# Kernel optimization log

Measured on AMD Instinct MI355X. Metric: run time of the kernel, lower is better.

## Reference

```python
import jax, jax.numpy as jnp
import numpy as np

S = 2   # upsample scale
K = 5   # reassembly kernel k_up


def setup_inputs() -> dict:
    key = jax.random.key(0)
    ks = jax.random.split(key, 7)
    B, C, H, W = 4, 128, 64, 64
    C_MID = 64
    return {
        "x": jax.random.normal(ks[0], (B, C, H, W), dtype=jnp.float32),
        "w1": jax.random.normal(ks[1], (C_MID, C), dtype=jnp.float32) * 0.05,
        "w2": jax.random.normal(ks[2], (S * S * K * K, C_MID, 3, 3), dtype=jnp.float32) * 0.05,
        "bn_gamma": jax.random.uniform(ks[3], (C_MID,), dtype=jnp.float32, minval=0.5, maxval=1.5),
        "bn_beta": jax.random.normal(ks[4], (C_MID,), dtype=jnp.float32) * 0.1,
        "bn_mean": jax.random.normal(ks[5], (C_MID,), dtype=jnp.float32) * 0.1,
        "bn_var": jax.random.uniform(ks[6], (C_MID,), dtype=jnp.float32, minval=0.5, maxval=1.5),
    }


def reference(x, w1, w2, bn_gamma, bn_beta, bn_mean, bn_var):
    B, C, H, W = x.shape
    s, k = S, K
    eps = 1e-5
    # --- content encoder: 1x1 conv -> BN (inference form) -> ReLU -> 3x3 conv ---
    h = jnp.einsum('bchw,oc->bohw', x, w1)  # (B, c_mid, H, W)
    inv = bn_gamma / jnp.sqrt(bn_var + eps)
    h = h * inv[None, :, None, None] + (bn_beta - bn_mean * inv)[None, :, None, None]
    h = jax.nn.relu(h)
    ker = jax.lax.conv_general_dilated(
        h, w2, window_strides=(1, 1), padding=((1, 1), (1, 1)),
        dimension_numbers=('NCHW', 'OIHW', 'NCHW'))  # (B, s*s*k*k, H, W)
    # softmax over the k*k reassembly window
    ker = jax.nn.softmax(ker.reshape(B, s * s, k * k, H, W), axis=2)
    # --- unfold k x k neighborhoods of x (row-major window order, as F.unfold) ---
    p = k // 2
    xp = jnp.pad(x, ((0, 0), (0, 0), (p, p), (p, p)))
    patches = jnp.stack(
        [xp[:, :, i:i + H, j:j + W] for i in range(k) for j in range(k)],
        axis=2)  # (B, C, k*k, H, W)
    # weighted reassembly: sum over the k*k window per (sub-pixel, channel)
    out = jnp.einsum('bckhw,bskhw->bcshw', patches, ker)  # (B, C, s*s, H, W)
    # pixel shuffle: (B, C, s, s, H, W) -> (B, C, H*s, W*s)
    out = out.reshape(B, C, s, s, H, W).transpose(0, 1, 4, 2, 5, 3)
    return out.reshape(B, C, H * s, W * s)
```

## Files before the change

kernel.cpp:

```cpp
#include <hip/hip_runtime.h>
#include <hip/hip_bf16.h>

#define HW 4096

typedef __attribute__((ext_vector_type(8))) short  short8;
typedef __attribute__((ext_vector_type(4))) float  floatx4;

#define OFF_W2B 0ul
#define OFF_W1B 129024ul
#define OFF_BN  145408ul
#define OFF_XG  145920ul

__device__ __forceinline__ float bfbits(unsigned u) {
    union { unsigned u; float f; } t; t.u = u; return t.f;
}

__global__ __launch_bounds__(256) void prep_kernel(const float* __restrict__ x,
                                                   const float* __restrict__ w1,
                                                   const float* __restrict__ w2,
                                                   const float* __restrict__ gamma,
                                                   const float* __restrict__ beta,
                                                   const float* __restrict__ mean,
                                                   const float* __restrict__ var,
                                                   char* __restrict__ ws) {
    int tid = blockIdx.x * 256 + threadIdx.x;
    if (tid < 262144) {
        int pix = tid & 4095;
        int cq  = (tid >> 12) & 15;
        int b   = tid >> 16;
        const float* xp = x + ((size_t)(b * 128 + cq * 8)) * HW + pix;
        union { short8 s; __hip_bfloat16 h[8]; } u;
        #pragma unroll
        for (int cc = 0; cc < 8; ++cc) u.h[cc] = __float2bfloat16(xp[(size_t)cc * HW]);
        *(short8*)((__hip_bfloat16*)(ws + OFF_XG) + (size_t)tid * 8) = u.s;
        return;
    }
    int t2 = tid - 262144;
    if (t2 < 64512) {
        int n = t2 / 576;
        int k = t2 - n * 576;
        int t = k >> 6, c = k & 63;
        float v = (n < 100) ? w2[(n * 64 + c) * 9 + t] : 0.f;
        ((__hip_bfloat16*)(ws + OFF_W2B))[t2] = __float2bfloat16(v);
    } else if (t2 < 64512 + 8192) {
        int i = t2 - 64512;
        ((__hip_bfloat16*)(ws + OFF_W1B))[i] = __float2bfloat16(w1[i]);
    } else if (t2 < 64512 + 8192 + 64) {
        int o = t2 - 64512 - 8192;
        float inv = gamma[o] * rsqrtf(var[o] + 1e-5f);
        ((float2*)(ws + OFF_BN))[o] = make_float2(inv, beta[o] - mean[o] * inv);
    }
}

__global__ __launch_bounds__(512, 4) void fused_carafe(const char* __restrict__ ws,
                                                       float* __restrict__ out) {
    __shared__ __align__(16) __hip_bfloat16 xs[1536 * 8];
    __shared__ __align__(16) __hip_bfloat16 hs[60 * 72];
    __shared__ __align__(16) float lg[32 * 114];
    __shared__ __align__(16) float ks[100 * 33];

    int b    = blockIdx.x >> 7;
    int tile = blockIdx.x & 127;
    int ty0 = (tile >> 3) * 4;
    int tx0 = (tile & 7) * 8;
    int tid = threadIdx.x;
    int lane = tid & 63, wave = tid >> 6;
    int q = lane >> 4, m = lane & 15;

    int bnt = wave & 3;
    int bo  = bnt * 16 + m;
    const __hip_bfloat16* w1b = (const __hip_bfloat16*)(ws + OFF_W1B);
    short8 bw[4];
    #pragma unroll
    for (int s = 0; s < 4; ++s)
        bw[s] = *(const short8*)(w1b + bo * 128 + s * 32 + q * 8);
    float2 bnia = ((const float2*)(ws + OFF_BN))[bo];

    const __hip_bfloat16* xg = (const __hip_bfloat16*)(ws + OFF_XG) + (size_t)b * 16 * 4096 * 8;
    #pragma unroll
    for (int it = 0; it < 3; ++it) {
        int idx = tid + it * 512;
        int cq = idx / 96, p = idx - cq * 96;
        int hy = p / 12, hx = p - hy * 12;
        int gy = ty0 + hy - 2, gx = tx0 + hx - 2;
        short8 v;
        #pragma unroll
        for (int j = 0; j < 8; ++j) v[j] = 0;
        if ((unsigned)gy < 64u && (unsigned)gx < 64u)
            v = *(const short8*)(xg + ((size_t)cq * 4096 + gy * 64 + gx) * 8);
        *(short8*)(&xs[idx * 8]) = v;
    }
    __syncthreads();

    #pragma unroll
    for (int mi = 0; mi < 2; ++mi) {
        int mt = (wave >> 2) * 2 + mi;
        int hp = mt * 16 + m;
        int hy1 = hp / 10, hx1 = hp - hy1 * 10;
        int xrow = (hy1 + 1) * 12 + (hx1 + 1);
        floatx4 acc;
        #pragma unroll
        for (int r = 0; r < 4; ++r) acc[r] = 0.f;
        #pragma unroll
        for (int s = 0; s < 4; ++s) {
            short8 a = *(const short8*)(&xs[((s * 4 + q) * 96 + xrow) * 8]);
            acc = __builtin_amdgcn_mfma_f32_16x16x32_bf16(a, bw[s], acc, 0, 0, 0);
        }
        #pragma unroll
        for (int r = 0; r < 4; ++r) {
            int prow = mt * 16 + q * 4 + r;
            if (prow < 60) {
                int phy = prow / 10, phx = prow - phy * 10;
                int gy = ty0 + phy - 1, gx = tx0 + phx - 1;
                bool in = ((unsigned)gy < 64u) && ((unsigned)gx < 64u);
                float v = in ? fmaxf(fmaf(acc[r], bnia.x, bnia.y), 0.f) : 0.f;
                hs[prow * 72 + bo] = __float2bfloat16(v);
            }
        }
    }
    __syncthreads();

    for (int task = wave; task < 14; task += 8) {
        int mt = task & 1, nt = task >> 1;
        int pixidx = mt * 16 + m;
        int py = pixidx >> 3, px = pixidx & 7;
        const __hip_bfloat16* w2b = (const __hip_bfloat16*)(ws + OFF_W2B);
        const __hip_bfloat16* bp  = w2b + (size_t)(nt * 16 + m) * 576 + q * 8;

        floatx4 acc;
        #pragma unroll
        for (int r = 0; r < 4; ++r) acc[r] = 0.f;

        short8 bcur = *(const short8*)bp;
        for (int s = 0; s < 18; ++s) {
            int t = s >> 1, c0 = (s & 1) * 32;
            int ti = t / 3, tj = t - ti * 3;
            short8 a = *(const short8*)(&hs[((py + ti) * 10 + px + tj) * 72 + c0 + q * 8]);
            short8 bn2 = bcur;
            if (s < 17) bn2 = *(const short8*)(bp + (s + 1) * 32);
            acc = __builtin_amdgcn_mfma_f32_16x16x32_bf16(a, bcur, acc, 0, 0, 0);
            bcur = bn2;
        }
        #pragma unroll
        for (int r = 0; r < 4; ++r)
            lg[(mt * 16 + q * 4 + r) * 114 + nt * 16 + m] = acc[r];
    }
    __syncthreads();

    if (tid < 128) {
        int pix = tid & 31, g = tid >> 5;
        float v[25];
        #pragma unroll
        for (int wi = 0; wi < 25; ++wi) v[wi] = lg[pix * 114 + g * 25 + wi];
        float mx = v[0];
        #pragma unroll
        for (int wi = 1; wi < 25; ++wi) mx = fmaxf(mx, v[wi]);
        float ssum = 0.f;
        #pragma unroll
        for (int wi = 0; wi < 25; ++wi) { v[wi] = __expf(v[wi] - mx); ssum += v[wi]; }
        float rs = 1.f / ssum;
        #pragma unroll
        for (int t25 = 0; t25 < 25; ++t25)
            ks[(t25 * 4 + g) * 33 + pix] = v[t25] * rs;
    }
    __syncthreads();

    {
        int pix   = lane & 31;
        int chunk = lane >> 5;
        int py = pix >> 3, px = pix & 7;
        int Y = ty0 + py, X = tx0 + px;

        for (int co = wave; co < 16; co += 8) {
            float acc[16];
            #pragma unroll
            for (int i = 0; i < 16; ++i) acc[i] = 0.f;

            const __hip_bfloat16* xsb = xs + (size_t)co * 96 * 8;
            #pragma unroll 5
            for (int t = 0; t < 25; ++t) {
                int ti = t / 5, tj = t - ti * 5;
                int xrow = (py + ti) * 12 + (px + tj);
                union { short8 s; unsigned u[4]; } xv;
                xv.s = *(const short8*)(xsb + xrow * 8);
                float k0 = ks[(t * 4 + chunk * 2 + 0) * 33 + pix];
                float k1 = ks[(t * 4 + chunk * 2 + 1) * 33 + pix];
                #pragma unroll
                for (int j = 0; j < 4; ++j) {
                    float xa  = bfbits(xv.u[j] << 16);
                    float xb2 = bfbits(xv.u[j] & 0xFFFF0000u);
                    acc[(j * 2 + 0) * 2 + 0] = fmaf(xa,  k0, acc[(j * 2 + 0) * 2 + 0]);
                    acc[(j * 2 + 0) * 2 + 1] = fmaf(xa,  k1, acc[(j * 2 + 0) * 2 + 1]);
                    acc[(j * 2 + 1) * 2 + 0] = fmaf(xb2, k0, acc[(j * 2 + 1) * 2 + 0]);
                    acc[(j * 2 + 1) * 2 + 1] = fmaf(xb2, k1, acc[(j * 2 + 1) * 2 + 1]);
                }
            }

            #pragma unroll
            for (int i = 0; i < 8; ++i) {
                size_t o0 = (((size_t)b * 128 + co * 8 + i) * 128 + 2 * Y + chunk) * 128 + 2 * X;
                *(float2*)(out + o0) = make_float2(acc[i * 2 + 0], acc[i * 2 + 1]);
            }
        }
    }
}

extern "C" void kernel_launch(void* const* d_in, const int* in_sizes, int n_in,
                              void* d_out, int out_size, void* d_ws, size_t ws_size,
                              hipStream_t stream) {
    const float* x     = (const float*)d_in[0];
    const float* w1    = (const float*)d_in[1];
    const float* w2    = (const float*)d_in[2];
    const float* gamma = (const float*)d_in[3];
    const float* beta  = (const float*)d_in[4];
    const float* mean  = (const float*)d_in[5];
    const float* var   = (const float*)d_in[6];
    float* out = (float*)d_out;
    char*  ws  = (char*)d_ws;

    prep_kernel<<<1309, 256, 0, stream>>>(x, w1, w2, gamma, beta, mean, var, ws);
    fused_carafe<<<512, 512, 0, stream>>>(ws, out);
}
```

Baseline: 102.2 us.

## Shrink output tile to 4x4, alias shared buffers, double blocks per CU

Changes the spatial tile from 4x8 to 4x4 pixels and launches 1024 blocks instead of 512. Shared memory is packed into one aliased buffer (hs and ks overlap) so occupancy can rise to 8 blocks per CU, and w1 fragments are loaded per task rather than held in registers. The output write changes from float2 pairs to scalar stores, with the sub-pixel split moved onto lanes. Smaller tiles raise halo recompute of the 1x1 and 3x3 convs and the x loads relative to useful work, and only 7 of 8 waves do the 3x3 MFMA stage.

```diff
diff --git a/kernel.cpp b/kernel.cpp
--- a/kernel.cpp
+++ b/kernel.cpp
@@ -52,78 +52,74 @@
     }
 }
 
-__global__ __launch_bounds__(512, 4) void fused_carafe(const char* __restrict__ ws,
+__global__ __launch_bounds__(512, 8) void fused_carafe(const char* __restrict__ ws,
                                                        float* __restrict__ out) {
-    __shared__ __align__(16) __hip_bfloat16 xs[1536 * 8];
-    __shared__ __align__(16) __hip_bfloat16 hs[60 * 72];
-    __shared__ __align__(16) float lg[32 * 114];
-    __shared__ __align__(16) float ks[100 * 33];
-
-    int b    = blockIdx.x >> 7;
-    int tile = blockIdx.x & 127;
-    int ty0 = (tile >> 3) * 4;
-    int tx0 = (tile & 7) * 8;
+    __shared__ __align__(16) char smem[30480];
+    __hip_bfloat16* xs = (__hip_bfloat16*)smem;
+    float*          lg = (float*)(smem + 16384);
+    __hip_bfloat16* hs = (__hip_bfloat16*)(smem + 23680);
+    float*          ks = (float*)(smem + 23680);
+
+    int b    = blockIdx.x >> 8;
+    int tile = blockIdx.x & 255;
+    int ty0 = (tile >> 4) * 4;
+    int tx0 = (tile & 15) * 4;
     int tid = threadIdx.x;
     int lane = tid & 63, wave = tid >> 6;
     int q = lane >> 4, m = lane & 15;
 
-    int bnt = wave & 3;
-    int bo  = bnt * 16 + m;
-    const __hip_bfloat16* w1b = (const __hip_bfloat16*)(ws + OFF_W1B);
-    short8 bw[4];
-    #pragma unroll
-    for (int s = 0; s < 4; ++s)
-        bw[s] = *(const short8*)(w1b + bo * 128 + s * 32 + q * 8);
-    float2 bnia = ((const float2*)(ws + OFF_BN))[bo];
-
     const __hip_bfloat16* xg = (const __hip_bfloat16*)(ws + OFF_XG) + (size_t)b * 16 * 4096 * 8;
     #pragma unroll
-    for (int it = 0; it < 3; ++it) {
+    for (int it = 0; it < 2; ++it) {
         int idx = tid + it * 512;
-        int cq = idx / 96, p = idx - cq * 96;
-        int hy = p / 12, hx = p - hy * 12;
-        int gy = ty0 + hy - 2, gx = tx0 + hx - 2;
+        int cq = idx >> 6, p = idx & 63;
+        int gy = ty0 + (p >> 3) - 2, gx = tx0 + (p & 7) - 2;
         short8 v;
         #pragma unroll
         for (int j = 0; j < 8; ++j) v[j] = 0;
         if ((unsigned)gy < 64u && (unsigned)gx < 64u)
             v = *(const short8*)(xg + ((size_t)cq * 4096 + gy * 64 + gx) * 8);
-        *(short8*)(&xs[idx * 8]) = v;
-    }
-    __syncthreads();
-
-    #pragma unroll
-    for (int mi = 0; mi < 2; ++mi) {
-        int mt = (wave >> 2) * 2 + mi;
-        int hp = mt * 16 + m;
-        int hy1 = hp / 10, hx1 = hp - hy1 * 10;
-        int xrow = (hy1 + 1) * 12 + (hx1 + 1);
-        floatx4 acc;
-        #pragma unroll
-        for (int r = 0; r < 4; ++r) acc[r] = 0.f;
-        #pragma unroll
-        for (int s = 0; s < 4; ++s) {
-            short8 a = *(const short8*)(&xs[((s * 4 + q) * 96 + xrow) * 8]);
-            acc = __builtin_amdgcn_mfma_f32_16x16x32_bf16(a, bw[s], acc, 0, 0, 0);
-        }
-        #pragma unroll
-        for (int r = 0; r < 4; ++r) {
-            int prow = mt * 16 + q * 4 + r;
-            if (prow < 60) {
-                int phy = prow / 10, phx = prow - phy * 10;
-                int gy = ty0 + phy - 1, gx = tx0 + phx - 1;
-                bool in = ((unsigned)gy < 64u) && ((unsigned)gx < 64u);
-                float v = in ? fmaxf(fmaf(acc[r], bnia.x, bnia.y), 0.f) : 0.f;
-                hs[prow * 72 + bo] = __float2bfloat16(v);
+        *(short8*)(xs + (size_t)idx * 8) = v;
+    }
+    __syncthreads();
+
+    {
+        const __hip_bfloat16* w1b = (const __hip_bfloat16*)(ws + OFF_W1B);
+        for (int task = wave; task < 12; task += 8) {
+            int mt = task >> 2, nt = task & 3;
+            int bo = nt * 16 + m;
+            float2 bnia = ((const float2*)(ws + OFF_BN))[bo];
+            int hp = mt * 16 + m;
+            int hpc = (hp < 36) ? hp : 0;
+            int hy1 = hpc / 6, hx1 = hpc - hy1 * 6;
+            int xrow = (hy1 + 1) * 8 + (hx1 + 1);
+            floatx4 acc;
+            #pragma unroll
+            for (int r = 0; r < 4; ++r) acc[r] = 0.f;
+            #pragma unroll
+            for (int s = 0; s < 4; ++s) {
+                short8 a  = *(const short8*)(xs + ((size_t)(s * 4 + q) * 64 + xrow) * 8);
+                short8 bw = *(const short8*)(w1b + bo * 128 + s * 32 + q * 8);
+                acc = __builtin_amdgcn_mfma_f32_16x16x32_bf16(a, bw, acc, 0, 0, 0);
+            }
+            #pragma unroll
+            for (int r = 0; r < 4; ++r) {
+                int prow = mt * 16 + q * 4 + r;
+                if (prow < 36) {
+                    int phy = prow / 6, phx = prow - phy * 6;
+                    int gy = ty0 + phy - 1, gx = tx0 + phx - 1;
+                    bool in = ((unsigned)gy < 64u) && ((unsigned)gx < 64u);
+                    float v = in ? fmaxf(fmaf(acc[r], bnia.x, bnia.y), 0.f) : 0.f;
+                    hs[prow * 72 + bo] = __float2bfloat16(v);
+                }
             }
         }
     }
     __syncthreads();
 
-    for (int task = wave; task < 14; task += 8) {
-        int mt = task & 1, nt = task >> 1;
-        int pixidx = mt * 16 + m;
-        int py = pixidx >> 3, px = pixidx & 7;
+    if (wave < 7) {
+        int nt = wave;
+        int py = m >> 2, px = m & 3;
         const __hip_bfloat16* w2b = (const __hip_bfloat16*)(ws + OFF_W2B);
         const __hip_bfloat16* bp  = w2b + (size_t)(nt * 16 + m) * 576 + q * 8;
 
@@ -135,7 +131,7 @@
         for (int s = 0; s < 18; ++s) {
             int t = s >> 1, c0 = (s & 1) * 32;
             int ti = t / 3, tj = t - ti * 3;
-            short8 a = *(const short8*)(&hs[((py + ti) * 10 + px + tj) * 72 + c0 + q * 8]);
+            short8 a = *(const short8*)(hs + ((size_t)((py + ti) * 6 + px + tj)) * 72 + c0 + q * 8);
             short8 bn2 = bcur;
             if (s < 17) bn2 = *(const short8*)(bp + (s + 1) * 32);
             acc = __builtin_amdgcn_mfma_f32_16x16x32_bf16(a, bcur, acc, 0, 0, 0);
@@ -143,12 +139,12 @@
         }
         #pragma unroll
         for (int r = 0; r < 4; ++r)
-            lg[(mt * 16 + q * 4 + r) * 114 + nt * 16 + m] = acc[r];
-    }
-    __syncthreads();
-
-    if (tid < 128) {
-        int pix = tid & 31, g = tid >> 5;
+            lg[(q * 4 + r) * 114 + nt * 16 + m] = acc[r];
+    }
+    __syncthreads();
+
+    if (tid < 64) {
+        int pix = tid & 15, g = tid >> 4;
         float v[25];
         #pragma unroll
         for (int wi = 0; wi < 25; ++wi) v[wi] = lg[pix * 114 + g * 25 + wi];
@@ -161,46 +157,42 @@
         float rs = 1.f / ssum;
         #pragma unroll
         for (int t25 = 0; t25 < 25; ++t25)
-            ks[(t25 * 4 + g) * 33 + pix] = v[t25] * rs;
+            ks[(t25 * 4 + g) * 17 + pix] = v[t25] * rs;
     }
     __syncthreads();
 
     {
-        int pix   = lane & 31;
-        int chunk = lane >> 5;
-        int py = pix >> 3, px = pix & 7;
+        int pix = lane & 15, g4 = lane >> 4;
+        int py = pix >> 2, px = pix & 3;
         int Y = ty0 + py, X = tx0 + px;
+        int gy = g4 >> 1, gx = g4 & 1;
+        float* op = out + ((((size_t)b * 128) * 128 + (2 * Y + gy)) * 128 + 2 * X + gx);
 
         for (int co = wave; co < 16; co += 8) {
-            float acc[16];
-            #pragma unroll
-            for (int i = 0; i < 16; ++i) acc[i] = 0.f;
-
-            const __hip_bfloat16* xsb = xs + (size_t)co * 96 * 8;
+            float acc[8];
+            #pragma unroll
+            for (int i = 0; i < 8; ++i) acc[i] = 0.f;
+
+            const __hip_bfloat16* xsb = xs + (size_t)co * 64 * 8;
             #pragma unroll 5
             for (int t = 0; t < 25; ++t) {
                 int ti = t / 5, tj = t - ti * 5;
-                int xrow = (py + ti) * 12 + (px + tj);
+                int xrow = (py + ti) * 8 + (px + tj);
                 union { short8 s; unsigned u[4]; } xv;
                 xv.s = *(const short8*)(xsb + xrow * 8);
-                float k0 = ks[(t * 4 + chunk * 2 + 0) * 33 + pix];
-                float k1 = ks[(t * 4 + chunk * 2 + 1) * 33 + pix];
+                float k = ks[(t * 4 + g4) * 17 + pix];
                 #pragma unroll
                 for (int j = 0; j < 4; ++j) {
                     float xa  = bfbits(xv.u[j] << 16);
                     float xb2 = bfbits(xv.u[j] & 0xFFFF0000u);
-                    acc[(j * 2 + 0) * 2 + 0] = fmaf(xa,  k0, acc[(j * 2 + 0) * 2 + 0]);
-                    acc[(j * 2 + 0) * 2 + 1] = fmaf(xa,  k1, acc[(j * 2 + 0) * 2 + 1]);
-                    acc[(j * 2 + 1) * 2 + 0] = fmaf(xb2, k0, acc[(j * 2 + 1) * 2 + 0]);
-                    acc[(j * 2 + 1) * 2 + 1] = fmaf(xb2, k1, acc[(j * 2 + 1) * 2 + 1]);
+                    acc[j * 2 + 0] = fmaf(xa,  k, acc[j * 2 + 0]);
+                    acc[j * 2 + 1] = fmaf(xb2, k, acc[j * 2 + 1]);
                 }
             }
 
             #pragma unroll
-            for (int i = 0; i < 8; ++i) {
-                size_t o0 = (((size_t)b * 128 + co * 8 + i) * 128 + 2 * Y + chunk) * 128 + 2 * X;
-                *(float2*)(out + o0) = make_float2(acc[i * 2 + 0], acc[i * 2 + 1]);
-            }
+            for (int i = 0; i < 8; ++i)
+                op[(size_t)(co * 8 + i) << 14] = acc[i];
         }
     }
 }
@@ -219,5 +211,5 @@
     char*  ws  = (char*)d_ws;
 
     prep_kernel<<<1309, 256, 0, stream>>>(x, w1, w2, gamma, beta, mean, var, ws);
-    fused_carafe<<<512, 512, 0, stream>>>(ws, out);
-}
+    fused_carafe<<<1024, 512, 0, stream>>>(ws, out);
+}
```

Result: slower. 117.0 us (+14.5%).
